# Performance work log

Measured on AMD Instinct MI355X. Metric: run time of the kernel, lower is better.

## Reference

```python
import jax, jax.numpy as jnp
import numpy as np

B, T, HD, HE = 32, 2048, 512, 1024
DH = 2 * HD  # flattened decoder hidden dim = 1024


def setup_inputs() -> dict:
    key = jax.random.key(0)
    k1, k2, k3, k4 = jax.random.split(key, 4)
    hidden = jax.random.normal(k1, (2, B, HD), dtype=jnp.float32)
    encoder_outputs = jax.random.normal(k2, (B, T, HE), dtype=jnp.float32)
    # valid-length mask: 1.0 for t < len, 0.0 after (lengths in [T//4, T])
    lens = jax.random.randint(k3, (B,), T // 4, T + 1)
    mask = (jnp.arange(T)[None, :] < lens[:, None]).astype(jnp.float32)
    W = jax.random.normal(k4, (1, DH + HE), dtype=jnp.float32) * (1.0 / np.sqrt(DH + HE))
    b = jnp.zeros((1,), dtype=jnp.float32)
    return {"hidden": hidden, "encoder_outputs": encoder_outputs, "mask": mask, "W": W, "b": b}


def reference(hidden, encoder_outputs, mask, W, b):
    # hidden: (layers*dirs, B, HD) -> (B, layers*dirs*HD)
    hid = jnp.transpose(hidden, (1, 0, 2)).reshape(B, -1)  # (B, DH)
    # Linear over concat(hidden_rep, enc_out) == two matvecs + broadcast add
    Wh = W[0, :DH]   # (DH,)
    We = W[0, DH:]   # (HE,)
    energies = jnp.einsum('bth,h->bt', encoder_outputs, We) + (hid @ Wh)[:, None] + b[0]  # (B,T)
    energies = energies * mask                     # mask BEFORE softmax (as in original)
    a = jax.nn.softmax(energies, axis=1)
    a = a * mask
    a = a / jnp.sum(a, axis=1, keepdims=True)      # renormalize
    context = jnp.einsum('bt,bth->bh', a, encoder_outputs)  # (B, HE)
    return context
```

## Files before the change

### kernel.cpp

```cpp
#include <hip/hip_runtime.h>
#include <cfloat>
#include <math.h>

#define B  32
#define T  2048
#define HD 512
#define HE 1024
#define DH 1024
#define NCMAX 16
#define G  8

__global__ __launch_bounds__(256) void k_hwh(const float* __restrict__ hidden,
                                             const float* __restrict__ W,
                                             const float* __restrict__ bvec,
                                             float* __restrict__ hwh) {
    const int b   = blockIdx.x;
    const int tid = threadIdx.x;
    const int i0  = tid * 4;
    const float* src = (i0 < HD) ? (hidden + (size_t)b * HD + i0)
                                 : (hidden + (size_t)B * HD + (size_t)b * HD + (i0 - HD));
    float4 h4 = *reinterpret_cast<const float4*>(src);
    float4 w4 = *reinterpret_cast<const float4*>(W + i0);
    float p = h4.x * w4.x + h4.y * w4.y + h4.z * w4.z + h4.w * w4.w;
    #pragma unroll
    for (int off = 32; off; off >>= 1) p += __shfl_xor(p, off);
    __shared__ float wsum[4];
    const int wave = tid >> 6, lane = tid & 63;
    if (lane == 0) wsum[wave] = p;
    __syncthreads();
    if (tid == 0) hwh[b] = wsum[0] + wsum[1] + wsum[2] + wsum[3] + bvec[0];
}

__global__ __launch_bounds__(256) void k_main(const float* __restrict__ enc,
                                              const float* __restrict__ mask,
                                              const float* __restrict__ W,
                                              const float* __restrict__ hwh,
                                              float* __restrict__ pctx,
                                              float* __restrict__ pm,
                                              float* __restrict__ ps,
                                              int nc) {
    const int bx  = blockIdx.x;
    const int b   = bx / nc;
    const int c   = bx % nc;
    const int tc  = T / nc;
    const int tid = threadIdx.x;
    const int wave = tid >> 6, lane = tid & 63;

    const float4 We4 = *reinterpret_cast<const float4*>(W + DH + tid * 4);
    const float  hb  = hwh[b];

    const float* encb  = enc  + (size_t)b * T * HE;
    const float* maskb = mask + (size_t)b * T;
    const int t0 = c * tc;

    float  m = -FLT_MAX;
    float  s = 0.f;
    float4 ctx = {0.f, 0.f, 0.f, 0.f};

    __shared__ float wpart[4][G];

    for (int g0 = 0; g0 < tc; g0 += G) {
        float4 v[G];
        float  p[G];
        #pragma unroll
        for (int g = 0; g < G; ++g) {
            const float* row = encb + (size_t)(t0 + g0 + g) * HE + tid * 4;
            v[g] = *reinterpret_cast<const float4*>(row);
            p[g] = v[g].x * We4.x + v[g].y * We4.y + v[g].z * We4.z + v[g].w * We4.w;
        }
        #pragma unroll
        for (int g = 0; g < G; ++g) {
            #pragma unroll
            for (int off = 32; off; off >>= 1) p[g] += __shfl_xor(p[g], off);
        }
        if (lane == 0) {
            #pragma unroll
            for (int g = 0; g < G; ++g) wpart[wave][g] = p[g];
        }
        __syncthreads();

        float e[G];
        float gm = -FLT_MAX;
        #pragma unroll
        for (int g = 0; g < G; ++g) {
            float eg = wpart[0][g] + wpart[1][g] + wpart[2][g] + wpart[3][g] + hb;
            float mk = maskb[t0 + g0 + g];
            e[g] = (mk > 0.5f) ? eg : -FLT_MAX;
            gm = fmaxf(gm, e[g]);
        }
        const float mn    = fmaxf(m, gm);
        const float scale = __expf(m - mn);
        float wsum = 0.f;
        float w[G];
        #pragma unroll
        for (int g = 0; g < G; ++g) {
            w[g] = (e[g] > -0.5f * FLT_MAX) ? __expf(e[g] - mn) : 0.f;
            wsum += w[g];
        }
        s = s * scale + wsum;
        ctx.x *= scale; ctx.y *= scale; ctx.z *= scale; ctx.w *= scale;
        #pragma unroll
        for (int g = 0; g < G; ++g) {
            ctx.x += w[g] * v[g].x;
            ctx.y += w[g] * v[g].y;
            ctx.z += w[g] * v[g].z;
            ctx.w += w[g] * v[g].w;
        }
        m = mn;
        __syncthreads();
    }

    *reinterpret_cast<float4*>(pctx + (size_t)bx * HE + tid * 4) = ctx;
    if (tid == 0) { pm[bx] = m; ps[bx] = s; }
}

__global__ __launch_bounds__(256) void k_combine(const float* __restrict__ pctx,
                                                 const float* __restrict__ pm,
                                                 const float* __restrict__ ps,
                                                 float* __restrict__ out,
                                                 int nc) {
    const int b   = blockIdx.x;
    const int tid = threadIdx.x;

    float M = -FLT_MAX;
    for (int c = 0; c < nc; ++c) M = fmaxf(M, pm[b * nc + c]);
    float S = 0.f;
    for (int c = 0; c < nc; ++c) {
        float mc = pm[b * nc + c];
        float f  = (mc > -0.5f * FLT_MAX) ? __expf(mc - M) : 0.f;
        S += f * ps[b * nc + c];
    }
    float4 acc = {0.f, 0.f, 0.f, 0.f};
    for (int c = 0; c < nc; ++c) {
        float mc = pm[b * nc + c];
        float f  = (mc > -0.5f * FLT_MAX) ? __expf(mc - M) : 0.f;
        float4 v = *reinterpret_cast<const float4*>(pctx + (size_t)(b * nc + c) * HE + tid * 4);
        acc.x += f * v.x; acc.y += f * v.y; acc.z += f * v.z; acc.w += f * v.w;
    }
    const float inv = 1.f / S;
    float4 o = {acc.x * inv, acc.y * inv, acc.z * inv, acc.w * inv};
    *reinterpret_cast<float4*>(out + (size_t)b * HE + tid * 4) = o;
}

extern "C" void kernel_launch(void* const* d_in, const int* in_sizes, int n_in,
                              void* d_out, int out_size, void* d_ws, size_t ws_size,
                              hipStream_t stream) {
    const float* hidden = (const float*)d_in[0];
    const float* enc    = (const float*)d_in[1];
    const float* mask   = (const float*)d_in[2];
    const float* W      = (const float*)d_in[3];
    const float* bvec   = (const float*)d_in[4];
    float* out = (float*)d_out;

    int nc = NCMAX;
    while (nc > 1) {
        size_t need = (size_t)B * nc * HE * sizeof(float)
                    + 2 * (size_t)B * nc * sizeof(float)
                    + 256;
        if (need <= ws_size) break;
        nc >>= 1;
    }

    char*  wsb  = (char*)d_ws;
    float* pctx = (float*)wsb;
    float* pm   = (float*)(wsb + (size_t)B * nc * HE * sizeof(float));
    float* ps   = pm + B * nc;
    float* hwh  = ps + B * nc;

    k_hwh   <<<B,      256, 0, stream>>>(hidden, W, bvec, hwh);
    k_main  <<<B * nc, 256, 0, stream>>>(enc, mask, W, hwh, pctx, pm, ps, nc);
    k_combine<<<B,     256, 0, stream>>>(pctx, pm, ps, out, nc);
}
```

Before: 376.9 us.

## Give each wave its own rows with a private online softmax, fold the hidden dot into the main kernel

Each of the four waves in a block now owns a contiguous run of rows and covers the full 1024-wide row itself, so energy reduction is a wave shuffle only. This removes the per-group shared-memory exchange and both __syncthreads. The hidden·Wh dot is computed inside each main block, which drops one kernel launch. The split grows to 32 chunks per batch with 4 partials each, so k_combine now reduces 128 partials per batch. The workspace-size fallback is removed, so the code assumes the workspace is large enough (about 16 MB of partials).

```diff
diff --git a/kernel.cpp b/kernel.cpp
--- a/kernel.cpp
+++ b/kernel.cpp
@@ -7,134 +7,139 @@
 #define HD 512
 #define HE 1024
 #define DH 1024
-#define NCMAX 16
-#define G  8
+#define NC 32
+#define TC (T / NC)
+#define WPB 4
+#define RPW (TC / WPB)
+#define RU 4
+#define NPART (NC * WPB)
 
-__global__ __launch_bounds__(256) void k_hwh(const float* __restrict__ hidden,
-                                             const float* __restrict__ W,
-                                             const float* __restrict__ bvec,
-                                             float* __restrict__ hwh) {
-    const int b   = blockIdx.x;
-    const int tid = threadIdx.x;
-    const int i0  = tid * 4;
-    const float* src = (i0 < HD) ? (hidden + (size_t)b * HD + i0)
-                                 : (hidden + (size_t)B * HD + (size_t)b * HD + (i0 - HD));
-    float4 h4 = *reinterpret_cast<const float4*>(src);
-    float4 w4 = *reinterpret_cast<const float4*>(W + i0);
-    float p = h4.x * w4.x + h4.y * w4.y + h4.z * w4.z + h4.w * w4.w;
-    #pragma unroll
-    for (int off = 32; off; off >>= 1) p += __shfl_xor(p, off);
-    __shared__ float wsum[4];
-    const int wave = tid >> 6, lane = tid & 63;
-    if (lane == 0) wsum[wave] = p;
-    __syncthreads();
-    if (tid == 0) hwh[b] = wsum[0] + wsum[1] + wsum[2] + wsum[3] + bvec[0];
-}
-
-__global__ __launch_bounds__(256) void k_main(const float* __restrict__ enc,
-                                              const float* __restrict__ mask,
-                                              const float* __restrict__ W,
-                                              const float* __restrict__ hwh,
-                                              float* __restrict__ pctx,
-                                              float* __restrict__ pm,
-                                              float* __restrict__ ps,
-                                              int nc) {
-    const int bx  = blockIdx.x;
-    const int b   = bx / nc;
-    const int c   = bx % nc;
-    const int tc  = T / nc;
-    const int tid = threadIdx.x;
+__global__ __launch_bounds__(256, 4) void k_main(const float* __restrict__ hidden,
+                                                 const float* __restrict__ enc,
+                                                 const float* __restrict__ mask,
+                                                 const float* __restrict__ W,
+                                                 const float* __restrict__ bvec,
+                                                 float* __restrict__ pctx,
+                                                 float* __restrict__ pm,
+                                                 float* __restrict__ ps) {
+    const int bx   = blockIdx.x;
+    const int b    = bx / NC;
+    const int c    = bx % NC;
+    const int tid  = threadIdx.x;
     const int wave = tid >> 6, lane = tid & 63;
 
-    const float4 We4 = *reinterpret_cast<const float4*>(W + DH + tid * 4);
-    const float  hb  = hwh[b];
+    __shared__ float red[WPB];
+    {
+        const int i0 = tid * 4;
+        const float* src = (i0 < HD) ? hidden + (size_t)b * HD + i0
+                                     : hidden + (size_t)(B + b) * HD + (i0 - HD);
+        float4 h4 = *reinterpret_cast<const float4*>(src);
+        float4 w4 = *reinterpret_cast<const float4*>(W + i0);
+        float p = h4.x * w4.x + h4.y * w4.y + h4.z * w4.z + h4.w * w4.w;
+        #pragma unroll
+        for (int off = 32; off; off >>= 1) p += __shfl_xor(p, off);
+        if (lane == 0) red[wave] = p;
+    }
+    __syncthreads();
+    const float hb = red[0] + red[1] + red[2] + red[3] + bvec[0];
+
+    float4 We4[4];
+    #pragma unroll
+    for (int j = 0; j < 4; ++j)
+        We4[j] = *reinterpret_cast<const float4*>(W + DH + lane * 4 + j * 256);
 
     const float* encb  = enc  + (size_t)b * T * HE;
     const float* maskb = mask + (size_t)b * T;
-    const int t0 = c * tc;
+    const int tbase = c * TC + wave * RPW;
 
-    float  m = -FLT_MAX;
-    float  s = 0.f;
-    float4 ctx = {0.f, 0.f, 0.f, 0.f};
+    float m = -FLT_MAX, s = 0.f;
+    float4 ctx[4];
+    #pragma unroll
+    for (int j = 0; j < 4; ++j) ctx[j] = make_float4(0.f, 0.f, 0.f, 0.f);
 
-    __shared__ float wpart[4][G];
-
-    for (int g0 = 0; g0 < tc; g0 += G) {
-        float4 v[G];
-        float  p[G];
+    for (int i = 0; i < RPW; i += RU) {
+        float4 v[RU][4];
+        float  p[RU], mk[RU];
         #pragma unroll
-        for (int g = 0; g < G; ++g) {
-            const float* row = encb + (size_t)(t0 + g0 + g) * HE + tid * 4;
-            v[g] = *reinterpret_cast<const float4*>(row);
-            p[g] = v[g].x * We4.x + v[g].y * We4.y + v[g].z * We4.z + v[g].w * We4.w;
+        for (int r = 0; r < RU; ++r) {
+            const float* row = encb + (size_t)(tbase + i + r) * HE + lane * 4;
+            #pragma unroll
+            for (int j = 0; j < 4; ++j)
+                v[r][j] = *reinterpret_cast<const float4*>(row + j * 256);
+            mk[r] = maskb[tbase + i + r];
         }
         #pragma unroll
-        for (int g = 0; g < G; ++g) {
+        for (int r = 0; r < RU; ++r) {
+            float acc = 0.f;
             #pragma unroll
-            for (int off = 32; off; off >>= 1) p[g] += __shfl_xor(p[g], off);
+            for (int j = 0; j < 4; ++j)
+                acc += v[r][j].x * We4[j].x + v[r][j].y * We4[j].y +
+                       v[r][j].z * We4[j].z + v[r][j].w * We4[j].w;
+            p[r] = acc;
         }
-        if (lane == 0) {
+        #pragma unroll
+        for (int r = 0; r < RU; ++r) {
             #pragma unroll
-            for (int g = 0; g < G; ++g) wpart[wave][g] = p[g];
+            for (int off = 32; off; off >>= 1) p[r] += __shfl_xor(p[r], off);
         }
-        __syncthreads();
-
-        float e[G];
-        float gm = -FLT_MAX;
+        float e[RU], gm = -FLT_MAX;
         #pragma unroll
-        for (int g = 0; g < G; ++g) {
-            float eg = wpart[0][g] + wpart[1][g] + wpart[2][g] + wpart[3][g] + hb;
-            float mk = maskb[t0 + g0 + g];
-            e[g] = (mk > 0.5f) ? eg : -FLT_MAX;
-            gm = fmaxf(gm, e[g]);
+        for (int r = 0; r < RU; ++r) {
+            e[r] = (mk[r] > 0.5f) ? p[r] + hb : -FLT_MAX;
+            gm = fmaxf(gm, e[r]);
         }
         const float mn    = fmaxf(m, gm);
         const float scale = __expf(m - mn);
-        float wsum = 0.f;
-        float w[G];
+        float w[RU], wsum = 0.f;
         #pragma unroll
-        for (int g = 0; g < G; ++g) {
-            w[g] = (e[g] > -0.5f * FLT_MAX) ? __expf(e[g] - mn) : 0.f;
-            wsum += w[g];
+        for (int r = 0; r < RU; ++r) {
+            w[r] = (e[r] > -0.5f * FLT_MAX) ? __expf(e[r] - mn) : 0.f;
+            wsum += w[r];
         }
         s = s * scale + wsum;
-        ctx.x *= scale; ctx.y *= scale; ctx.z *= scale; ctx.w *= scale;
         #pragma unroll
-        for (int g = 0; g < G; ++g) {
-            ctx.x += w[g] * v[g].x;
-            ctx.y += w[g] * v[g].y;
-            ctx.z += w[g] * v[g].z;
-            ctx.w += w[g] * v[g].w;
+        for (int j = 0; j < 4; ++j) {
+            ctx[j].x *= scale; ctx[j].y *= scale; ctx[j].z *= scale; ctx[j].w *= scale;
+            #pragma unroll
+            for (int r = 0; r < RU; ++r) {
+                ctx[j].x += w[r] * v[r][j].x;
+                ctx[j].y += w[r] * v[r][j].y;
+                ctx[j].z += w[r] * v[r][j].z;
+                ctx[j].w += w[r] * v[r][j].w;
+            }
         }
         m = mn;
-        __syncthreads();
     }
 
-    *reinterpret_cast<float4*>(pctx + (size_t)bx * HE + tid * 4) = ctx;
-    if (tid == 0) { pm[bx] = m; ps[bx] = s; }
+    const int part = bx * WPB + wave;
+    float* pc = pctx + (size_t)part * HE + lane * 4;
+    #pragma unroll
+    for (int j = 0; j < 4; ++j)
+        *reinterpret_cast<float4*>(pc + j * 256) = ctx[j];
+    if (lane == 0) { pm[part] = m; ps[part] = s; }
 }
 
 __global__ __launch_bounds__(256) void k_combine(const float* __restrict__ pctx,
                                                  const float* __restrict__ pm,
                                                  const float* __restrict__ ps,
-                                                 float* __restrict__ out,
-                                                 int nc) {
+                                                 float* __restrict__ out) {
     const int b   = blockIdx.x;
     const int tid = threadIdx.x;
+    const int p0  = b * NPART;
 
     float M = -FLT_MAX;
-    for (int c = 0; c < nc; ++c) M = fmaxf(M, pm[b * nc + c]);
+    for (int c = 0; c < NPART; ++c) M = fmaxf(M, pm[p0 + c]);
     float S = 0.f;
-    for (int c = 0; c < nc; ++c) {
-        float mc = pm[b * nc + c];
+    for (int c = 0; c < NPART; ++c) {
+        float mc = pm[p0 + c];
         float f  = (mc > -0.5f * FLT_MAX) ? __expf(mc - M) : 0.f;
-        S += f * ps[b * nc + c];
+        S += f * ps[p0 + c];
     }
     float4 acc = {0.f, 0.f, 0.f, 0.f};
-    for (int c = 0; c < nc; ++c) {
-        float mc = pm[b * nc + c];
+    for (int c = 0; c < NPART; ++c) {
+        float mc = pm[p0 + c];
         float f  = (mc > -0.5f * FLT_MAX) ? __expf(mc - M) : 0.f;
-        float4 v = *reinterpret_cast<const float4*>(pctx + (size_t)(b * nc + c) * HE + tid * 4);
+        float4 v = *reinterpret_cast<const float4*>(pctx + (size_t)(p0 + c) * HE + tid * 4);
         acc.x += f * v.x; acc.y += f * v.y; acc.z += f * v.z; acc.w += f * v.w;
     }
     const float inv = 1.f / S;
@@ -152,22 +157,11 @@
     const float* bvec   = (const float*)d_in[4];
     float* out = (float*)d_out;
 
-    int nc = NCMAX;
-    while (nc > 1) {
-        size_t need = (size_t)B * nc * HE * sizeof(float)
-                    + 2 * (size_t)B * nc * sizeof(float)
-                    + 256;
-        if (need <= ws_size) break;
-        nc >>= 1;
-    }
-
     char*  wsb  = (char*)d_ws;
     float* pctx = (float*)wsb;
-    float* pm   = (float*)(wsb + (size_t)B * nc * HE * sizeof(float));
-    float* ps   = pm + B * nc;
-    float* hwh  = ps + B * nc;
+    float* pm   = (float*)(wsb + (size_t)B * NPART * HE * sizeof(float));
+    float* ps   = pm + B * NPART;
 
-    k_hwh   <<<B,      256, 0, stream>>>(hidden, W, bvec, hwh);
-    k_main  <<<B * nc, 256, 0, stream>>>(enc, mask, W, hwh, pctx, pm, ps, nc);
-    k_combine<<<B,     256, 0, stream>>>(pctx, pm, ps, out, nc);
+    k_main   <<<B * NC, 256, 0, stream>>>(hidden, enc, mask, W, bvec, pctx, pm, ps);
+    k_combine<<<B,      256, 0, stream>>>(pctx, pm, ps, out);
 }
```

Result: slower. 391.8 us (+4.0%).
